# Performance work log

Hardware: AMD Instinct MI355X
Metric: run time of the kernel (lower is better)

The kernel has to match this reference:

```python
import jax, jax.numpy as jnp
import numpy as np

NUM_GROUPS = 16
GN_EPS = 1e-5
POOL = 4
CLAMP_MIN, CLAMP_MAX = 0.0, 1.0


def setup_inputs() -> dict:
    key = jax.random.key(0)
    k = jax.random.split(key, 4)
    x = jax.random.normal(k[0], (128, 8, 128, 128), dtype=jnp.float32)
    conv_weight = jax.random.normal(k[1], (64, 8, 3, 3), dtype=jnp.float32) * 0.1
    conv_bias = jax.random.normal(k[2], (64,), dtype=jnp.float32) * 0.1
    gn_weight = jnp.ones((64,), dtype=jnp.float32)
    gn_bias = jnp.zeros((64,), dtype=jnp.float32)
    scale = jax.random.normal(k[3], (64, 1, 1), dtype=jnp.float32)
    return {"x": x, "conv_weight": conv_weight, "conv_bias": conv_bias,
            "gn_weight": gn_weight, "gn_bias": gn_bias, "scale": scale}


def reference(x, conv_weight, conv_bias, gn_weight, gn_bias, scale):
    # Conv2d 3x3, stride 1, padding 0 (torch defaults). NCHW / OIHW.
    y = jax.lax.conv_general_dilated(
        x, conv_weight, window_strides=(1, 1), padding='VALID',
        dimension_numbers=('NCHW', 'OIHW', 'NCHW'))
    y = y + conv_bias[None, :, None, None]  # [N, 64, 126, 126]

    # GroupNorm(16 groups over 64 channels): stats over (C//G, H, W) per group.
    N, C, H, W = y.shape
    g = y.reshape(N, NUM_GROUPS, C // NUM_GROUPS, H, W)
    mean = jnp.mean(g, axis=(2, 3, 4), keepdims=True)
    var = jnp.mean(jnp.square(g - mean), axis=(2, 3, 4), keepdims=True)
    g = (g - mean) * jax.lax.rsqrt(var + GN_EPS)
    y = g.reshape(N, C, H, W) * gn_weight[None, :, None, None] + gn_bias[None, :, None, None]

    # Per-channel scale (scale has shape [64, 1, 1], broadcasts over H, W).
    y = y * scale[None]

    # MaxPool2d(kernel=4, stride=4), floor mode -> 126 // 4 = 31.
    y = jax.lax.reduce_window(
        y, -jnp.inf, jax.lax.max,
        window_dimensions=(1, 1, POOL, POOL),
        window_strides=(1, 1, POOL, POOL), padding='VALID')

    # Clamp.
    return jnp.clip(y, CLAMP_MIN, CLAMP_MAX)
```

## Files before the change

### kernel.cpp

```cpp
#include <hip/hip_runtime.h>
#include <hip/hip_fp16.h>

namespace {
constexpr int ICH = 8, IH = 128, IW = 128;
constexpr int CPG = 4, PH = 31;
constexpr int ICS = 516;
constexpr float EPS = 1e-5f;
constexpr float MPX = 126.f * 126.f;
constexpr int TOTAL_OUT = 128 * 64 * PH * PH;
constexpr size_t XH_BYTES = (size_t)128 * 128 * 128 * 8 * 2;
constexpr size_t WS_NEED = XH_BYTES + (size_t)128 * 16 * 8 * 2 * 4;

typedef _Float16 v8h __attribute__((ext_vector_type(8)));
typedef float v4f __attribute__((ext_vector_type(4)));
typedef unsigned short u16;
typedef unsigned int u32;

__device__ __forceinline__ void gll16(const void* g, void* l) {
  __builtin_amdgcn_global_load_lds((const __attribute__((address_space(1))) void*)g,
                                   (__attribute__((address_space(3))) void*)l, 16, 0, 0);
}

__device__ __forceinline__ u32 pkh(float a, float b) {
  unsigned short lo = __half_as_ushort(__float2half_rn(a));
  unsigned short hi = __half_as_ushort(__float2half_rn(b));
  return (u32)lo | ((u32)hi << 16);
}

__global__ __launch_bounds__(256) void pack_f16x8(const float* __restrict__ x,
                                                  u16* __restrict__ xh) {
  int i = blockIdx.x * 256 + threadIdx.x;
  int n = i >> 14, rc = i & 16383;
  const float* bp = x + ((size_t)n << 17) + rc;
  uint4 o;
  o.x = pkh(bp[0],      bp[16384]);
  o.y = pkh(bp[32768],  bp[49152]);
  o.z = pkh(bp[65536],  bp[81920]);
  o.w = pkh(bp[98304],  bp[114688]);
  *reinterpret_cast<uint4*>(xh + (size_t)i * 8) = o;
}

__global__ __launch_bounds__(256, 2) void conv_mfma(
    const u16* __restrict__ xh, const float* __restrict__ cw,
    const float* __restrict__ cb, const float* __restrict__ gnw,
    const float* __restrict__ sc, float* __restrict__ out,
    float* __restrict__ wsp) {
  __shared__ __align__(16) u16 ring[12][1056];

  const int bid = blockIdx.x;
  const int n = bid >> 3, e = bid & 7;
  const int out_lo = e * 16;
  const int out_hi = (e == 7) ? 125 : out_lo + 15;
  const int NST = (e == 7) ? 4 : 5;
  const int t = threadIdx.x;
  const int w = t >> 6, l = t & 63;
  const int colB = l & 15, qt = l >> 4;

  for (int idx = t; idx < 12 * 32; idx += 256)
    ring[idx >> 5][1024 + (idx & 31)] = 0;

  const int ocA = 16 * w + colB;
  const float flipA = (gnw[ocA] * sc[ocA] >= 0.f) ? 1.f : -1.f;
  v8h af[3];
#pragma unroll
  for (int kc = 0; kc < 3; ++kc) {
    const int tap = kc * 4 + qt;
#pragma unroll
    for (int i = 0; i < 8; ++i)
      af[kc][i] = (tap < 9) ? (_Float16)(flipA * cw[ocA * 72 + i * 9 + tap])
                            : (_Float16)0.f;
  }
  int eofc[3], dhl[3];
#pragma unroll
  for (int kc = 0; kc < 3; ++kc) {
    int tap = kc * 4 + qt; tap = (tap > 8) ? 8 : tap;
    dhl[kc] = tap / 3;
    eofc[kc] = (colB + tap % 3) * 8;
  }
  float flip[4];
#pragma unroll
  for (int q = 0; q < 4; ++q) {
    int oc = 16 * w + qt * 4 + q;
    flip[q] = (gnw[oc] * sc[oc] >= 0.f) ? 1.f : -1.f;
  }
  const u16* rb = &ring[0][0];

  auto issue = [&](int s) {
#pragma unroll
    for (int k = 0; k < 2; ++k) {
      int mk = w * 2 + k;
      int grow = out_lo + 4 * s + (mk >> 1);
      int hv = mk & 1;
      int slot = grow % 12;
      gll16(xh + ((size_t)(n * 128 + grow) * 128 + hv * 64) * 8 + l * 8,
            (void*)&ring[slot][hv * 512]);
    }
  };

  issue(0);

  float s1q[4] = {0.f, 0.f, 0.f, 0.f};
  float s2g = 0.f;
  float pacc[8][4];
#pragma unroll
  for (int ci = 0; ci < 8; ++ci)
#pragma unroll
    for (int q = 0; q < 4; ++q) pacc[ci][q] = -3.4e38f;

  for (int s = 0; s < NST; ++s) {
    __syncthreads();
    if (s + 1 < NST) issue(s + 1);
#pragma unroll
    for (int ri = 0; ri < 4; ++ri) {
      const int r = out_lo + 4 * s - 2 + ri;
      if (r < out_lo || r > out_hi) continue;
      const int rm = r % 12;
      int eoff[3];
#pragma unroll
      for (int kc = 0; kc < 3; ++kc) {
        int sl = rm + dhl[kc];
        if (sl >= 12) sl -= 12;
        eoff[kc] = sl * 1056 + eofc[kc];
      }
#pragma unroll
      for (int ci = 0; ci < 8; ++ci) {
        v4f acc = {0.f, 0.f, 0.f, 0.f};
#pragma unroll
        for (int kc = 0; kc < 3; ++kc) {
          v8h bf = *reinterpret_cast<const v8h*>(rb + eoff[kc] + ci * 128);
          acc = __builtin_amdgcn_mfma_f32_16x16x32_f16(af[kc], bf, acc, 0, 0, 0);
        }
        if (ci < 7) {
#pragma unroll
          for (int q = 0; q < 4; ++q) {
            s1q[q] += acc[q];
            s2g = fmaf(acc[q], acc[q], s2g);
            pacc[ci][q] = fmaxf(pacc[ci][q], acc[q]);
          }
        } else {
          const bool va = (colB < 14);
#pragma unroll
          for (int q = 0; q < 4; ++q) {
            float a = va ? acc[q] : 0.f;
            s1q[q] += a;
            s2g = fmaf(a, a, s2g);
            float fv = va ? acc[q] : -3.4e38f;
            pacc[7][q] = fmaxf(pacc[7][q], fv);
          }
        }
      }
      if ((r & 3) == 3) {
        const int pr = r >> 2;
        float* ob = out + (((size_t)n * 64 + 16 * w + qt * 4) * PH + pr) * PH;
#pragma unroll
        for (int ci = 0; ci < 8; ++ci) {
#pragma unroll
          for (int q = 0; q < 4; ++q) {
            float pm = pacc[ci][q];
            pm = fmaxf(pm, __shfl_xor(pm, 1, 64));
            pm = fmaxf(pm, __shfl_xor(pm, 2, 64));
            if ((l & 3) == 0 && (ci < 7 || colB < 12)) {
              int pc = ci * 4 + (colB >> 2);
              ob[(size_t)q * (PH * PH) + pc] = flip[q] * pm;
            }
            pacc[ci][q] = -3.4e38f;
          }
        }
      }
    }
  }

#pragma unroll
  for (int off = 1; off <= 8; off <<= 1) {
#pragma unroll
    for (int q = 0; q < 4; ++q) s1q[q] += __shfl_xor(s1q[q], off, 64);
    s2g += __shfl_xor(s2g, off, 64);
  }
  if ((l & 15) == 0) {
    const float cnte = 126.f * (float)(out_hi - out_lo + 1);
    float S1 = 0.f, S2 = s2g;
#pragma unroll
    for (int q = 0; q < 4; ++q) {
      float s1t = flip[q] * s1q[q];
      float b = cb[16 * w + qt * 4 + q];
      S1 += s1t + cnte * b;
      S2 += 2.f * b * s1t + cnte * b * b;
    }
    int g = 4 * w + qt;
    float* wp = wsp + ((size_t)(n * 16 + g) * 8 + e) * 2;
    wp[0] = S1; wp[1] = S2;
  }
}

__global__ __launch_bounds__(256) void gn_affine_clamp(
    float* __restrict__ out, const float* __restrict__ wsp,
    const float* __restrict__ gnw, const float* __restrict__ gnb,
    const float* __restrict__ sc, const float* __restrict__ cb) {
  int i = blockIdx.x * 256 + threadIdx.x;
  const int stride = gridDim.x * 256;
  for (; i < TOTAL_OUT; i += stride) {
    int c = (i / 961) & 63;
    int n = i / 61504;
    const float* wp = wsp + ((size_t)(n * 16 + (c >> 2)) * 8) * 2;
    float S1 = 0.f, S2 = 0.f;
#pragma unroll
    for (int e = 0; e < 8; ++e) { S1 += wp[2 * e]; S2 += wp[2 * e + 1]; }
    constexpr float invN = 1.f / (4.f * MPX);
    float mean = S1 * invN;
    float var = S2 * invN - mean * mean;
    float inv = rsqrtf(var + EPS);
    float gw = gnw[c];
    float A = gw * inv * sc[c];
    float B = (gnb[c] - mean * inv * gw) * sc[c] + A * cb[c];
    float v = fmaf(A, out[i], B);
    out[i] = fminf(fmaxf(v, 0.f), 1.f);
  }
}

#define FIN(T, DOSTATS, RE)                                                    \
  {                                                                            \
    float f0 = T[0] + __shfl_xor(T[0], 32, 64);                                \
    float f1 = T[1] + __shfl_xor(T[1], 32, 64);                                \
    float f2 = T[2] + __shfl_xor(T[2], 32, 64);                                \
    float f3 = T[3] + __shfl_xor(T[3], 32, 64);                                \
    if (DOSTATS) {                                                             \
      s1 += f0 + f1 + m23 * (f2 + f3);                                         \
      float qa = fmaf(f0, f0, f1 * f1);                                        \
      float qb = fmaf(f2, f2, f3 * f3);                                        \
      s2 += qa + m23 * qb;                                                     \
    }                                                                          \
    RE = fmaxf(fmaxf(flip * f0, flip * f1), fmaxf(flip * f2, flip * f3));      \
  }
#define ZERO(T) { T[0] = 0.f; T[1] = 0.f; T[2] = 0.f; T[3] = 0.f; }
#define ROWF(RR, T2, T1, T0)                                                   \
  {                                                                            \
    _Pragma("unroll") for (int i4 = 0; i4 < 4; ++i4) {                         \
      const float* rp = bp + (4 * p + i4) * ICS + (RR) * IW + 4 * j;           \
      float4 v4 = *reinterpret_cast<const float4*>(rp);                        \
      float2 v2 = *reinterpret_cast<const float2*>(rp + 4);                    \
      float in[6] = {v4.x, v4.y, v4.z, v4.w, v2.x, v2.y};                      \
      _Pragma("unroll") for (int dw = 0; dw < 3; ++dw) {                       \
        const float w0 = wf[i4 * 9 + dw];                                      \
        const float w1 = wf[i4 * 9 + 3 + dw];                                  \
        const float w2 = wf[i4 * 9 + 6 + dw];                                  \
        _Pragma("unroll") for (int q = 0; q < 4; ++q) {                        \
          T2[q] = fmaf(in[q + dw], w2, T2[q]);                                 \
          T1[q] = fmaf(in[q + dw], w1, T1[q]);                                 \
          T0[q] = fmaf(in[q + dw], w0, T0[q]);                                 \
        }                                                                      \
      }                                                                        \
    }                                                                          \
  }
#define STAGEF(S, X, Y, Z, DOS01, DOWIN)                                       \
  {                                                                            \
    __syncthreads();                                                           \
    const int cur = (S) & 1;                                                   \
    if ((S) < 31) issue(4 * ((S) + 1), cur ^ 1);                               \
    const float* bp = &buf[cur][0][0];                                         \
    float re0, re1, re2, re3;                                                  \
    ROWF(0, X, Y, Z) FIN(X, DOS01, re0) ZERO(X)                                \
    ROWF(1, Y, Z, X) FIN(Y, DOS01, re1) ZERO(Y)                                \
    if (DOWIN) {                                                               \
      float wfin = fmaxf(wprev, fmaxf(re0, re1));                              \
      if (p == 0 && j < 31) mm[c][(S) - 1][j] = __float2half(flip * wfin);     \
    }                                                                          \
    ROWF(2, Z, X, Y) FIN(Z, true, re2) ZERO(Z)                                 \
    ROWF(3, X, Y, Z) FIN(X, true, re3) ZERO(X)                                 \
    wprev = fmaxf(re2, re3);                                                   \
  }

__global__ __launch_bounds__(256, 2) void fused_conv_gn_pool_f32(
    const float* __restrict__ x, const float* __restrict__ cw,
    const float* __restrict__ cb, const float* __restrict__ gnw,
    const float* __restrict__ gnb, const float* __restrict__ sc,
    float* __restrict__ out) {
  __shared__ float buf[2][ICH][ICS];
  __shared__ __half mm[CPG][PH][PH];
  __shared__ float red[8];
  __shared__ float stats[2];

  const int bid = blockIdx.x;
  const int xcd = bid & 7;
  const int kb = bid >> 3;
  const int n = xcd * 16 + (kb >> 4);
  const int g = kb & 15;
  const int t = threadIdx.x;
  const int c = t >> 6;
  const int u = t & 63;
  const int p = u >> 5;
  const int j = u & 31;
  const int gc = g * CPG + c;

  float wf[36];
  {
    const float4* wp = reinterpret_cast<const float4*>(cw + gc * 72 + p * 36);
#pragma unroll
    for (int q = 0; q < 9; ++q) {
      float4 v = wp[q];
      wf[4 * q + 0] = v.x; wf[4 * q + 1] = v.y;
      wf[4 * q + 2] = v.z; wf[4 * q + 3] = v.w;
    }
  }
  const float flip = ((gnw[gc] * sc[gc]) >= 0.f) ? 1.f : -1.f;
  const float m23 = (j < 31) ? 1.f : 0.f;

  const float* xn = x + (size_t)n * ICH * IH * IW;

  auto issue = [&](int br, int which) {
#pragma unroll
    for (int k = 0; k < 4; ++k) {
      const int m = c * 4 + k;
      const int ic = m >> 1;
      const int r2 = (m & 1) * 2;
      const float* gp = xn + (size_t)(ic * IH + br + r2) * IW + u * 4;
      gll16(gp, &buf[which][ic][r2 * IW]);
    }
  };

  issue(0, 0);

  float s1 = 0.f, s2 = 0.f, wprev = 0.f;
  float A0[4] = {0, 0, 0, 0}, A1[4] = {0, 0, 0, 0}, A2[4] = {0, 0, 0, 0};

  STAGEF(0, A0, A1, A2, false, false)
  for (int s = 1; s <= 28; s += 3) {
    STAGEF(s,     A1, A2, A0, true, true)
    STAGEF(s + 1, A2, A0, A1, true, true)
    STAGEF(s + 2, A0, A1, A2, true, true)
  }
  STAGEF(31, A1, A2, A0, true, true)

#pragma unroll
  for (int off = 32; off > 0; off >>= 1) {
    s1 += __shfl_down(s1, off, 64);
    s2 += __shfl_down(s2, off, 64);
  }
  const float bc = cb[gc];
  if (u == 0) {
    float t1 = 0.5f * s1, t2 = 0.5f * s2;
    red[c * 2] = t1 + MPX * bc;
    red[c * 2 + 1] = t2 + 2.f * bc * t1 + MPX * bc * bc;
  }
  __syncthreads();
  if (t == 0) {
    float S1 = red[0] + red[2] + red[4] + red[6];
    float S2 = red[1] + red[3] + red[5] + red[7];
    constexpr float invN = 1.f / (CPG * 126.f * 126.f);
    float mean = S1 * invN;
    float var = S2 * invN - mean * mean;
    stats[0] = mean;
    stats[1] = rsqrtf(var + EPS);
  }
  __syncthreads();
  const float mean = stats[0], inv = stats[1];

  float* outp = out + ((size_t)n * 64 + g * CPG) * (PH * PH);
  for (int kk = 0; kk < 16; ++kk) {
    int idx = t + kk * 256;
    if (idx < CPG * PH * PH) {
      int cc = idx / (PH * PH);
      int rem = idx - cc * (PH * PH);
      float e = __half2float(mm[cc][rem / PH][rem % PH]);
      int gcc = g * CPG + cc;
      float gw = gnw[gcc];
      float A = gw * inv * sc[gcc];
      float B = (gnb[gcc] - mean * inv * gw) * sc[gcc] + A * cb[gcc];
      float v = fmaf(A, e, B);
      v = fminf(fmaxf(v, 0.f), 1.f);
      outp[cc * (PH * PH) + rem] = v;
    }
  }
}
}

extern "C" void kernel_launch(void* const* d_in, const int* in_sizes, int n_in,
                              void* d_out, int out_size, void* d_ws, size_t ws_size,
                              hipStream_t stream) {
  const float* x   = (const float*)d_in[0];
  const float* cw  = (const float*)d_in[1];
  const float* cb  = (const float*)d_in[2];
  const float* gnw = (const float*)d_in[3];
  const float* gnb = (const float*)d_in[4];
  const float* sc  = (const float*)d_in[5];
  float* out = (float*)d_out;

  if (ws_size >= WS_NEED) {
    u16* xh = (u16*)d_ws;
    float* wsp = (float*)((char*)d_ws + XH_BYTES);
    hipLaunchKernelGGL(pack_f16x8, dim3(8192), dim3(256), 0, stream, x, xh);
    hipLaunchKernelGGL(conv_mfma, dim3(1024), dim3(256), 0, stream,
                       xh, cw, cb, gnw, sc, out, wsp);
    hipLaunchKernelGGL(gn_affine_clamp, dim3(2048), dim3(256), 0, stream,
                       out, wsp, gnw, gnb, sc, cb);
  } else {
    hipLaunchKernelGGL(fused_conv_gn_pool_f32, dim3(2048), dim3(256), 0, stream,
                       x, cw, cb, gnw, gnb, sc, out);
  }
}
```

Measured before the change: 99.33 us.

## Fuse fp16 packing into conv kernel via register-prefetched global loads

Drops the separate pack kernel that converted the fp32 input to an fp16 channel-interleaved layout in workspace. The conv kernel now reads fp32 rows straight from global memory into registers at the start of each stage, then converts and writes them into the LDS ring after that stage's compute. This removes a full fp16 write and re-read of the input and one kernel launch. In exchange, halo rows are read again at fp32 width, register pressure rises, and the async global-to-LDS loads become synchronous register loads.

```diff
diff --git a/kernel.cpp b/kernel.cpp
--- a/kernel.cpp
+++ b/kernel.cpp
@@ -8,8 +8,7 @@
 constexpr float EPS = 1e-5f;
 constexpr float MPX = 126.f * 126.f;
 constexpr int TOTAL_OUT = 128 * 64 * PH * PH;
-constexpr size_t XH_BYTES = (size_t)128 * 128 * 128 * 8 * 2;
-constexpr size_t WS_NEED = XH_BYTES + (size_t)128 * 16 * 8 * 2 * 4;
+constexpr size_t WS_NEED = (size_t)128 * 16 * 8 * 2 * 4;
 
 typedef _Float16 v8h __attribute__((ext_vector_type(8)));
 typedef float v4f __attribute__((ext_vector_type(4)));
@@ -27,21 +26,8 @@
   return (u32)lo | ((u32)hi << 16);
 }
 
-__global__ __launch_bounds__(256) void pack_f16x8(const float* __restrict__ x,
-                                                  u16* __restrict__ xh) {
-  int i = blockIdx.x * 256 + threadIdx.x;
-  int n = i >> 14, rc = i & 16383;
-  const float* bp = x + ((size_t)n << 17) + rc;
-  uint4 o;
-  o.x = pkh(bp[0],      bp[16384]);
-  o.y = pkh(bp[32768],  bp[49152]);
-  o.z = pkh(bp[65536],  bp[81920]);
-  o.w = pkh(bp[98304],  bp[114688]);
-  *reinterpret_cast<uint4*>(xh + (size_t)i * 8) = o;
-}
-
 __global__ __launch_bounds__(256, 2) void conv_mfma(
-    const u16* __restrict__ xh, const float* __restrict__ cw,
+    const float* __restrict__ x, const float* __restrict__ cw,
     const float* __restrict__ cb, const float* __restrict__ gnw,
     const float* __restrict__ sc, float* __restrict__ out,
     float* __restrict__ wsp) {
@@ -85,19 +71,36 @@
   }
   const u16* rb = &ring[0][0];
 
-  auto issue = [&](int s) {
-#pragma unroll
-    for (int k = 0; k < 2; ++k) {
-      int mk = w * 2 + k;
-      int grow = out_lo + 4 * s + (mk >> 1);
-      int hv = mk & 1;
-      int slot = grow % 12;
-      gll16(xh + ((size_t)(n * 128 + grow) * 128 + hv * 64) * 8 + l * 8,
-            (void*)&ring[slot][hv * 512]);
+  const int prg = t >> 7;
+  const int px = t & 127;
+  const float* xb = x + ((size_t)n * ICH) * (IH * IW) + px;
+  float fs[16];
+  auto load_regs = [&](int s) {
+#pragma unroll
+    for (int rr = 0; rr < 2; ++rr) {
+      const int grow = out_lo + 4 * s + 2 * prg + rr;
+      const float* gp = xb + (size_t)grow * IW;
+#pragma unroll
+      for (int ic = 0; ic < 8; ++ic)
+        fs[rr * 8 + ic] = gp[(size_t)ic * (IH * IW)];
     }
   };
-
-  issue(0);
+  auto write_lds = [&](int s) {
+#pragma unroll
+    for (int rr = 0; rr < 2; ++rr) {
+      const int grow = out_lo + 4 * s + 2 * prg + rr;
+      const int slot = grow % 12;
+      uint4 v;
+      v.x = pkh(fs[rr * 8 + 0], fs[rr * 8 + 1]);
+      v.y = pkh(fs[rr * 8 + 2], fs[rr * 8 + 3]);
+      v.z = pkh(fs[rr * 8 + 4], fs[rr * 8 + 5]);
+      v.w = pkh(fs[rr * 8 + 6], fs[rr * 8 + 7]);
+      *reinterpret_cast<uint4*>(&ring[slot][px * 8]) = v;
+    }
+  };
+
+  load_regs(0);
+  write_lds(0);
 
   float s1q[4] = {0.f, 0.f, 0.f, 0.f};
   float s2g = 0.f;
@@ -109,7 +112,7 @@
 
   for (int s = 0; s < NST; ++s) {
     __syncthreads();
-    if (s + 1 < NST) issue(s + 1);
+    if (s + 1 < NST) load_regs(s + 1);
 #pragma unroll
     for (int ri = 0; ri < 4; ++ri) {
       const int r = out_lo + 4 * s - 2 + ri;
@@ -168,6 +171,7 @@
         }
       }
     }
+    if (s + 1 < NST) write_lds(s + 1);
   }
 
 #pragma unroll
@@ -385,11 +389,9 @@
   float* out = (float*)d_out;
 
   if (ws_size >= WS_NEED) {
-    u16* xh = (u16*)d_ws;
-    float* wsp = (float*)((char*)d_ws + XH_BYTES);
-    hipLaunchKernelGGL(pack_f16x8, dim3(8192), dim3(256), 0, stream, x, xh);
+    float* wsp = (float*)d_ws;
     hipLaunchKernelGGL(conv_mfma, dim3(1024), dim3(256), 0, stream,
-                       xh, cw, cb, gnw, sc, out, wsp);
+                       x, cw, cb, gnw, sc, out, wsp);
     hipLaunchKernelGGL(gn_affine_clamp, dim3(2048), dim3(256), 0, stream,
                        out, wsp, gnw, gnb, sc, cb);
   } else {
```

Result: faster. 91.63 us (-7.7%).
